# Optimization experiments

Measured on AMD Instinct MI355X. Metric: run time of the kernel, lower is better.

Reference implementation:

```python
import jax, jax.numpy as jnp
import numpy as np

N = 50000      # nodes
E = 800000     # edges (avg degree 16)
IN = 128       # in_features
H = 4          # num_heads
OUT = 32       # out_features per head
NEG_SLOPE = 0.2


def setup_inputs() -> dict:
    key = jax.random.key(0)
    k1, k2, k3, k4 = jax.random.split(key, 4)
    h = jax.random.normal(k1, (N, IN), dtype=jnp.float32)
    edge_index = jax.random.randint(k2, (2, E), 0, N, dtype=jnp.int32)
    # xavier-ish init scales
    W = jax.random.normal(k3, (H, IN, OUT), dtype=jnp.float32) * np.float32(np.sqrt(2.0 / (IN + OUT)))
    a = jax.random.normal(k4, (H, 2 * OUT), dtype=jnp.float32) * np.float32(np.sqrt(2.0 / (2 * OUT)))
    return {"h": h, "edge_index": edge_index, "W": W, "a": a}


def reference(h, edge_index, W, a):
    src, dst = edge_index[0], edge_index[1]
    # project per head: [N, H, OUT]
    h_proj = jnp.einsum('ni,hio->nho', h, W)
    # score = leaky_relu(a . [Wh_src || Wh_dst]) ; split a to avoid materializing the concat
    a_src, a_dst = a[:, :OUT], a[:, OUT:]
    s_src = jnp.einsum('nho,ho->nh', h_proj, a_src)   # [N, H]
    s_dst = jnp.einsum('nho,ho->nh', h_proj, a_dst)   # [N, H]
    score = jax.nn.leaky_relu(s_src[src] + s_dst[dst], negative_slope=NEG_SLOPE)  # [E, H]
    # sparse softmax over incoming edges of each dst node
    smax = jax.ops.segment_max(score, dst, num_segments=N)          # [N, H]
    smax = jnp.where(jnp.isfinite(smax), smax, jnp.float32(-1e9))   # nodes with no in-edges
    score_exp = jnp.exp(score - smax[dst])                          # [E, H]
    denom = jax.ops.segment_sum(score_exp, dst, num_segments=N)     # [N, H]
    denom = jnp.maximum(denom, jnp.float32(1e-16))
    alpha = score_exp / denom[dst]                                  # [E, H]
    # weighted aggregation (dropout is identity in eval mode)
    h_src = h_proj[src]                                             # [E, H, OUT]
    h_out = jax.ops.segment_sum(alpha[:, :, None] * h_src, dst, num_segments=N)  # [N, H, OUT]
    h_out = h_out.reshape(N, H * OUT)  # concat=True
    return jax.nn.elu(h_out)
```

## Files before the change

kernel.cpp:

```cpp
#include <hip/hip_runtime.h>

#define NEG_SLOPE 0.2f

typedef __attribute__((ext_vector_type(8))) short short8;
typedef __attribute__((ext_vector_type(4))) float floatx4;

__device__ __forceinline__ unsigned f2bf(float x) {
  unsigned u = __float_as_uint(x);
  unsigned r = ((u >> 16) & 1u) + 0x7fffu;
  return (u + r) >> 16;
}
__device__ __forceinline__ float bf2f(unsigned hi16) {
  return __uint_as_float(hi16 << 16);
}

__global__ __launch_bounds__(256) void k_prep(const float* __restrict__ W,
                                              uint4* __restrict__ gWf) {
  const int u = blockIdx.x * 256 + threadIdx.x;
  if (u >= 2048) return;
  int ln = u & 63;
  int kc = (u >> 6) & 3;
  int ct = u >> 8;
  int n = ct * 16 + (ln & 15);
  int kb = kc * 32 + (ln >> 4) * 8;
  int head = n >> 5;
  const float* src = W + head * 4096 + (size_t)kb * 32 + (n & 31);
  unsigned hi[4], lo[4];
#pragma unroll
  for (int jj = 0; jj < 4; ++jj) {
    float w0 = src[(2 * jj) * 32];
    float w1 = src[(2 * jj + 1) * 32];
    unsigned h0 = f2bf(w0), h1 = f2bf(w1);
    unsigned l0 = f2bf(w0 - bf2f(h0)), l1 = f2bf(w1 - bf2f(h1));
    hi[jj] = h0 | (h1 << 16);
    lo[jj] = l0 | (l1 << 16);
  }
  gWf[u] = make_uint4(hi[0], hi[1], hi[2], hi[3]);
  gWf[2048 + u] = make_uint4(lo[0], lo[1], lo[2], lo[3]);
}

__global__ __launch_bounds__(256) void k_gemm(const float* __restrict__ h,
                                              const uint4* __restrict__ gWf,
                                              const float* __restrict__ a,
                                              unsigned short* __restrict__ hp16,
                                              float* __restrict__ ssrc,
                                              float* __restrict__ sdst, int N) {
  __shared__ unsigned lds_u[16384];
  const int tid = threadIdx.x;
  const int lane = tid & 63;
  const int wv = tid >> 6;
  const int quad = lane >> 4;
  const int l16 = lane & 15;

  for (int u = tid; u < 4096; u += 256)
    *(uint4*)&lds_u[u * 4] = gWf[u];

  const int row0 = blockIdx.x * 64;
  const int r = row0 + wv * 16 + l16;
  short8 Ah[4], Al[4];
#pragma unroll
  for (int kc = 0; kc < 4; ++kc) {
    float v[8];
    if (r < N) {
      float4 fa = *(const float4*)&h[(size_t)r * 128 + kc * 32 + quad * 8];
      float4 fb = *(const float4*)&h[(size_t)r * 128 + kc * 32 + quad * 8 + 4];
      v[0] = fa.x; v[1] = fa.y; v[2] = fa.z; v[3] = fa.w;
      v[4] = fb.x; v[5] = fb.y; v[6] = fb.z; v[7] = fb.w;
    } else {
#pragma unroll
      for (int j = 0; j < 8; ++j) v[j] = 0.f;
    }
#pragma unroll
    for (int j = 0; j < 8; ++j) {
      unsigned hi = f2bf(v[j]);
      Ah[kc][j] = (short)hi;
      Al[kc][j] = (short)f2bf(v[j] - bf2f(hi));
    }
  }
  __syncthreads();

  floatx4 C[8];
#pragma unroll
  for (int ct = 0; ct < 8; ++ct) {
    floatx4 c = {0.f, 0.f, 0.f, 0.f};
#pragma unroll
    for (int kc = 0; kc < 4; ++kc) {
      int bidx = ((ct * 4 + kc) * 64 + lane) * 4;
      short8 Bh, Bl;
      *(uint4*)&Bh = *(const uint4*)&lds_u[bidx];
      *(uint4*)&Bl = *(const uint4*)&lds_u[8192 + bidx];
      c = __builtin_amdgcn_mfma_f32_16x16x32_bf16(Ah[kc], Bh, c, 0, 0, 0);
      c = __builtin_amdgcn_mfma_f32_16x16x32_bf16(Al[kc], Bh, c, 0, 0, 0);
      c = __builtin_amdgcn_mfma_f32_16x16x32_bf16(Ah[kc], Bl, c, 0, 0, 0);
    }
    C[ct] = c;
  }
  __syncthreads();

  float* epi = (float*)lds_u;
#pragma unroll
  for (int ct = 0; ct < 8; ++ct) {
#pragma unroll
    for (int reg = 0; reg < 4; ++reg) {
      int rr = wv * 16 + quad * 4 + reg;
      epi[rr * 132 + ct * 16 + l16] = C[ct][reg];
    }
  }
  __syncthreads();

  const int row_l = tid >> 2;
  const int hh = tid & 3;
  const int rg = row0 + row_l;
  if (rg < N) {
    const float* rowp = &epi[row_l * 132 + hh * 32];
    float ss = 0.f, sd = 0.f;
    unsigned pka[16];
#pragma unroll
    for (int e = 0; e < 8; ++e) {
      float4 c4 = *(const float4*)&rowp[e * 4];
      float4 as = *(const float4*)&a[hh * 64 + e * 4];
      float4 ad = *(const float4*)&a[hh * 64 + 32 + e * 4];
      ss += c4.x * as.x + c4.y * as.y + c4.z * as.z + c4.w * as.w;
      sd += c4.x * ad.x + c4.y * ad.y + c4.z * ad.z + c4.w * ad.w;
      pka[e * 2] = f2bf(c4.x) | (f2bf(c4.y) << 16);
      pka[e * 2 + 1] = f2bf(c4.z) | (f2bf(c4.w) << 16);
    }
    unsigned short* dst = &hp16[(size_t)rg * 128 + hh * 32];
    *(uint4*)(dst) = make_uint4(pka[0], pka[1], pka[2], pka[3]);
    *(uint4*)(dst + 8) = make_uint4(pka[4], pka[5], pka[6], pka[7]);
    *(uint4*)(dst + 16) = make_uint4(pka[8], pka[9], pka[10], pka[11]);
    *(uint4*)(dst + 24) = make_uint4(pka[12], pka[13], pka[14], pka[15]);
    ssrc[(size_t)rg * 4 + hh] = ss;
    sdst[(size_t)rg * 4 + hh] = sd;
  }
}

__global__ __launch_bounds__(256) void k_count(const int* __restrict__ ei,
                                               int* __restrict__ gcntT,
                                               int E, int NB1, int NB2) {
  __shared__ int cnt[256];
  const int tid = threadIdx.x;
  const int e0 = blockIdx.x * 4096;
  for (int i = tid; i < NB2; i += 256) cnt[i] = 0;
  __syncthreads();
#pragma unroll
  for (int j = 0; j < 16; ++j) {
    int e = e0 + j * 256 + tid;
    if (e < E) atomicAdd(&cnt[ei[E + e] >> 8], 1);
  }
  __syncthreads();
  for (int i = tid; i < NB2; i += 256)
    gcntT[(size_t)i * NB1 + blockIdx.x] = cnt[i];
}

__global__ __launch_bounds__(256) void k_scan_col(int* __restrict__ gcntT,
                                                  int* __restrict__ btot, int NB1) {
  __shared__ int lds[256];
  const int tid = threadIdx.x;
  int* col = gcntT + (size_t)blockIdx.x * NB1;
  int carry = 0;
  for (int base = 0; base < NB1; base += 256) {
    int i = base + tid;
    int v = (i < NB1) ? col[i] : 0;
    lds[tid] = v;
    __syncthreads();
    for (int off = 1; off < 256; off <<= 1) {
      int t = (tid >= off) ? lds[tid - off] : 0;
      __syncthreads();
      lds[tid] += t;
      __syncthreads();
    }
    if (i < NB1) col[i] = carry + lds[tid] - v;
    carry += lds[255];
    __syncthreads();
  }
  if (tid == 0) btot[blockIdx.x] = carry;
}

__global__ __launch_bounds__(256) void k_scan_bk(const int* __restrict__ btot,
                                                 int* __restrict__ bbase, int NB2, int E) {
  __shared__ int lds[256];
  const int tid = threadIdx.x;
  int s = (tid < NB2) ? btot[tid] : 0;
  lds[tid] = s;
  __syncthreads();
  for (int off = 1; off < 256; off <<= 1) {
    int t = (tid >= off) ? lds[tid - off] : 0;
    __syncthreads();
    lds[tid] += t;
    __syncthreads();
  }
  if (tid < NB2) {
    bbase[tid] = lds[tid] - s;
    if (tid == NB2 - 1) bbase[NB2] = E;
  }
}

__global__ __launch_bounds__(256) void k_bin(const int* __restrict__ ei,
                                             const int* __restrict__ gcntT,
                                             const int* __restrict__ bbase,
                                             uint2* __restrict__ gpairs,
                                             int E, int NB1, int NB2) {
  __shared__ uint2 stage[4096];
  __shared__ int cnt[256], start[256], cur[256], gbase[256];
  const int tid = threadIdx.x;
  const int e0 = blockIdx.x * 4096;
  for (int i = tid; i < NB2; i += 256) cnt[i] = 0;
  __syncthreads();
  int sarr[16], darr[16];
#pragma unroll
  for (int j = 0; j < 16; ++j) {
    int e = e0 + j * 256 + tid;
    if (e < E) {
      sarr[j] = ei[e];
      darr[j] = ei[E + e];
      atomicAdd(&cnt[darr[j] >> 8], 1);
    } else {
      darr[j] = -1;
    }
  }
  __syncthreads();
  {
    int s = (tid < NB2) ? cnt[tid] : 0;
    __shared__ int lds[256];
    lds[tid] = s;
    __syncthreads();
    for (int off = 1; off < 256; off <<= 1) {
      int t = (tid >= off) ? lds[tid - off] : 0;
      __syncthreads();
      lds[tid] += t;
      __syncthreads();
    }
    if (tid < NB2) {
      start[tid] = lds[tid] - s;
      cur[tid] = lds[tid] - s;
      gbase[tid] = gcntT[(size_t)tid * NB1 + blockIdx.x] + bbase[tid];
    }
  }
  __syncthreads();
#pragma unroll
  for (int j = 0; j < 16; ++j) {
    if (darr[j] >= 0) {
      int b = darr[j] >> 8;
      int pos = atomicAdd(&cur[b], 1);
      stage[pos] = make_uint2((unsigned)sarr[j], (unsigned)darr[j]);
    }
  }
  __syncthreads();
  const int total = start[NB2 - 1] + cnt[NB2 - 1];
  for (int u = tid; u < total; u += 256) {
    uint2 pr = stage[u];
    int b = (int)(pr.y >> 8);
    gpairs[gbase[b] + (u - start[b])] = pr;
  }
}

__global__ __launch_bounds__(256) void k_build(const int* __restrict__ bbase,
                                               const uint2* __restrict__ gpairs,
                                               int* __restrict__ csr_src,
                                               int* __restrict__ offs, int N) {
  __shared__ int cnt2[256], start2[256], cur2[256];
  __shared__ int srcsort[8192];
  const int tid = threadIdx.x;
  const int b = blockIdx.x;
  const int base = bbase[b];
  const int size = bbase[b + 1] - base;
  const int d0 = b << 8;
  const int ndst = min(256, N - d0);
  cnt2[tid] = 0;
  __syncthreads();
  for (int u = tid; u < size; u += 256)
    atomicAdd(&cnt2[(int)gpairs[base + u].y - d0], 1);
  __syncthreads();
  {
    int s = cnt2[tid];
    __shared__ int lds[256];
    lds[tid] = s;
    __syncthreads();
    for (int off = 1; off < 256; off <<= 1) {
      int t = (tid >= off) ? lds[tid - off] : 0;
      __syncthreads();
      lds[tid] += t;
      __syncthreads();
    }
    start2[tid] = lds[tid] - s;
    cur2[tid] = lds[tid] - s;
  }
  __syncthreads();
  for (int u = tid; u < size; u += 256) {
    uint2 pr = gpairs[base + u];
    int pos = atomicAdd(&cur2[(int)pr.y - d0], 1);
    srcsort[pos] = (int)pr.x;
  }
  __syncthreads();
  for (int u = tid; u < size; u += 256) csr_src[base + u] = srcsort[u];
  if (tid < ndst) offs[d0 + tid] = base + start2[tid] + cnt2[tid];
}

__global__ __launch_bounds__(256) void k_agg(const int* __restrict__ offs,
                                             const int* __restrict__ csr_src,
                                             const float* __restrict__ ssrc,
                                             const float* __restrict__ sdst,
                                             const uint4* __restrict__ hp4,
                                             float* __restrict__ out, int N) {
  const int t = blockIdx.x * 256 + threadIdx.x;
  const int d = t >> 4;
  if (d >= N) return;
  const int l = threadIdx.x & 15;
  const int hh = l >> 2;
  const int beg = (d == 0) ? 0 : offs[d - 1];
  const int end = offs[d];
  const float sdh = sdst[(size_t)d * 4 + hh];

  float den0 = 0.f, den1 = 0.f;
  float acc[8];
#pragma unroll
  for (int j = 0; j < 8; ++j) acc[j] = 0.f;

  int p = beg;
  for (; p + 1 < end; p += 2) {
    int s0 = csr_src[p];
    int s1 = csr_src[p + 1];
    float sc0 = ssrc[(size_t)s0 * 4 + hh] + sdh;
    float sc1 = ssrc[(size_t)s1 * 4 + hh] + sdh;
    uint4 v0 = hp4[(size_t)s0 * 16 + l];
    uint4 v1 = hp4[(size_t)s1 * 16 + l];
    sc0 = sc0 >= 0.f ? sc0 : NEG_SLOPE * sc0;
    sc1 = sc1 >= 0.f ? sc1 : NEG_SLOPE * sc1;
    float w0 = __expf(sc0);
    float w1 = __expf(sc1);
    den0 += w0;
    den1 += w1;
    acc[0] = fmaf(w0, bf2f(v0.x & 0xffffu), acc[0]);
    acc[1] = fmaf(w0, bf2f(v0.x >> 16), acc[1]);
    acc[2] = fmaf(w0, bf2f(v0.y & 0xffffu), acc[2]);
    acc[3] = fmaf(w0, bf2f(v0.y >> 16), acc[3]);
    acc[4] = fmaf(w0, bf2f(v0.z & 0xffffu), acc[4]);
    acc[5] = fmaf(w0, bf2f(v0.z >> 16), acc[5]);
    acc[6] = fmaf(w0, bf2f(v0.w & 0xffffu), acc[6]);
    acc[7] = fmaf(w0, bf2f(v0.w >> 16), acc[7]);
    acc[0] = fmaf(w1, bf2f(v1.x & 0xffffu), acc[0]);
    acc[1] = fmaf(w1, bf2f(v1.x >> 16), acc[1]);
    acc[2] = fmaf(w1, bf2f(v1.y & 0xffffu), acc[2]);
    acc[3] = fmaf(w1, bf2f(v1.y >> 16), acc[3]);
    acc[4] = fmaf(w1, bf2f(v1.z & 0xffffu), acc[4]);
    acc[5] = fmaf(w1, bf2f(v1.z >> 16), acc[5]);
    acc[6] = fmaf(w1, bf2f(v1.w & 0xffffu), acc[6]);
    acc[7] = fmaf(w1, bf2f(v1.w >> 16), acc[7]);
  }
  if (p < end) {
    int s0 = csr_src[p];
    float sc0 = ssrc[(size_t)s0 * 4 + hh] + sdh;
    uint4 v0 = hp4[(size_t)s0 * 16 + l];
    sc0 = sc0 >= 0.f ? sc0 : NEG_SLOPE * sc0;
    float w0 = __expf(sc0);
    den0 += w0;
    acc[0] = fmaf(w0, bf2f(v0.x & 0xffffu), acc[0]);
    acc[1] = fmaf(w0, bf2f(v0.x >> 16), acc[1]);
    acc[2] = fmaf(w0, bf2f(v0.y & 0xffffu), acc[2]);
    acc[3] = fmaf(w0, bf2f(v0.y >> 16), acc[3]);
    acc[4] = fmaf(w0, bf2f(v0.z & 0xffffu), acc[4]);
    acc[5] = fmaf(w0, bf2f(v0.z >> 16), acc[5]);
    acc[6] = fmaf(w0, bf2f(v0.w & 0xffffu), acc[6]);
    acc[7] = fmaf(w0, bf2f(v0.w >> 16), acc[7]);
  }
  float rden = 1.f / fmaxf(den0 + den1, 1e-16f);
  float o[8];
#pragma unroll
  for (int j = 0; j < 8; ++j) {
    float x = acc[j] * rden;
    o[j] = x > 0.f ? x : expm1f(x);
  }
  float* dst = &out[(size_t)d * 128 + l * 8];
  *(float4*)dst = make_float4(o[0], o[1], o[2], o[3]);
  *(float4*)(dst + 4) = make_float4(o[4], o[5], o[6], o[7]);
}

extern "C" void kernel_launch(void* const* d_in, const int* in_sizes, int n_in,
                              void* d_out, int out_size, void* d_ws, size_t ws_size,
                              hipStream_t stream) {
  const float* h = (const float*)d_in[0];
  const int* ei = (const int*)d_in[1];
  const float* W = (const float*)d_in[2];
  const float* a = (const float*)d_in[3];
  float* out = (float*)d_out;
  const int N = in_sizes[0] / 128;
  const int E = in_sizes[1] / 2;
  const int NB2 = (N + 255) >> 8;
  const int NB1 = (E + 4095) / 4096;

  char* ws = (char*)d_ws;
  uint4* gWf = (uint4*)ws;
  unsigned short* hp16 = (unsigned short*)(gWf + 4096);
  uint2* gpairs = (uint2*)(hp16 + (size_t)N * 128);
  float* ssrc = (float*)(gpairs + (size_t)E);
  float* sdst = ssrc + (size_t)N * 4;
  int* gcntT = (int*)(sdst + (size_t)N * 4);
  int* btot = gcntT + (size_t)NB2 * NB1;
  int* bbase = btot + NB2;
  int* offs = bbase + NB2 + 1;
  int* csr_src = offs + N;

  k_prep<<<8, 256, 0, stream>>>(W, gWf);
  k_gemm<<<(N + 63) / 64, 256, 0, stream>>>(h, gWf, a, hp16, ssrc, sdst, N);
  k_count<<<NB1, 256, 0, stream>>>(ei, gcntT, E, NB1, NB2);
  k_scan_col<<<NB2, 256, 0, stream>>>(gcntT, btot, NB1);
  k_scan_bk<<<1, 256, 0, stream>>>(btot, bbase, NB2, E);
  k_bin<<<NB1, 256, 0, stream>>>(ei, gcntT, bbase, gpairs, E, NB1, NB2);
  k_build<<<NB2, 256, 0, stream>>>(bbase, gpairs, csr_src, offs, N);
  k_agg<<<(N * 16 + 255) / 256, 256, 0, stream>>>(offs, csr_src, ssrc, sdst,
                                                  (const uint4*)hp16, out, N);
}
```

Baseline: 167.3 us.

## Fuse edge counting into GEMM, inline bucket scan, unroll aggregation by four

The per-bucket destination counting moves into the first NB1 blocks of the GEMM kernel, and the single-block bucket-base scan kernel is removed. k_bin and k_build now each recompute that scan redundantly from btot. This cuts two launches and their serialization gaps, at the cost of extra scan work in every block and a longer GEMM prologue in some blocks. The aggregation loop is unrolled from two to four edges, with four denominator partials, to put more independent gathers in flight.

```diff
diff --git a/kernel.cpp b/kernel.cpp
--- a/kernel.cpp
+++ b/kernel.cpp
@@ -42,11 +42,30 @@
 __global__ __launch_bounds__(256) void k_gemm(const float* __restrict__ h,
                                               const uint4* __restrict__ gWf,
                                               const float* __restrict__ a,
+                                              const int* __restrict__ ei,
                                               unsigned short* __restrict__ hp16,
                                               float* __restrict__ ssrc,
-                                              float* __restrict__ sdst, int N) {
+                                              float* __restrict__ sdst,
+                                              int* __restrict__ gcntT,
+                                              int N, int E, int NB1, int NB2) {
   __shared__ unsigned lds_u[16384];
+  __shared__ int cnt[256];
   const int tid = threadIdx.x;
+
+  if (blockIdx.x < NB1) {
+    for (int i = tid; i < NB2; i += 256) cnt[i] = 0;
+    __syncthreads();
+    const int e0 = blockIdx.x * 4096;
+#pragma unroll
+    for (int j = 0; j < 16; ++j) {
+      int e = e0 + j * 256 + tid;
+      if (e < E) atomicAdd(&cnt[ei[E + e] >> 8], 1);
+    }
+    __syncthreads();
+    for (int i = tid; i < NB2; i += 256)
+      gcntT[(size_t)i * NB1 + blockIdx.x] = cnt[i];
+  }
+
   const int lane = tid & 63;
   const int wv = tid >> 6;
   const int quad = lane >> 4;
@@ -133,24 +152,6 @@
     ssrc[(size_t)rg * 4 + hh] = ss;
     sdst[(size_t)rg * 4 + hh] = sd;
   }
-}
-
-__global__ __launch_bounds__(256) void k_count(const int* __restrict__ ei,
-                                               int* __restrict__ gcntT,
-                                               int E, int NB1, int NB2) {
-  __shared__ int cnt[256];
-  const int tid = threadIdx.x;
-  const int e0 = blockIdx.x * 4096;
-  for (int i = tid; i < NB2; i += 256) cnt[i] = 0;
-  __syncthreads();
-#pragma unroll
-  for (int j = 0; j < 16; ++j) {
-    int e = e0 + j * 256 + tid;
-    if (e < E) atomicAdd(&cnt[ei[E + e] >> 8], 1);
-  }
-  __syncthreads();
-  for (int i = tid; i < NB2; i += 256)
-    gcntT[(size_t)i * NB1 + blockIdx.x] = cnt[i];
 }
 
 __global__ __launch_bounds__(256) void k_scan_col(int* __restrict__ gcntT,
@@ -177,34 +178,26 @@
   if (tid == 0) btot[blockIdx.x] = carry;
 }
 
-__global__ __launch_bounds__(256) void k_scan_bk(const int* __restrict__ btot,
-                                                 int* __restrict__ bbase, int NB2, int E) {
-  __shared__ int lds[256];
-  const int tid = threadIdx.x;
-  int s = (tid < NB2) ? btot[tid] : 0;
-  lds[tid] = s;
-  __syncthreads();
-  for (int off = 1; off < 256; off <<= 1) {
-    int t = (tid >= off) ? lds[tid - off] : 0;
-    __syncthreads();
-    lds[tid] += t;
-    __syncthreads();
-  }
-  if (tid < NB2) {
-    bbase[tid] = lds[tid] - s;
-    if (tid == NB2 - 1) bbase[NB2] = E;
-  }
-}
-
 __global__ __launch_bounds__(256) void k_bin(const int* __restrict__ ei,
                                              const int* __restrict__ gcntT,
-                                             const int* __restrict__ bbase,
+                                             const int* __restrict__ btot,
                                              uint2* __restrict__ gpairs,
                                              int E, int NB1, int NB2) {
   __shared__ uint2 stage[4096];
   __shared__ int cnt[256], start[256], cur[256], gbase[256];
+  __shared__ int lds[256];
   const int tid = threadIdx.x;
   const int e0 = blockIdx.x * 4096;
+  int bt = (tid < NB2) ? btot[tid] : 0;
+  lds[tid] = bt;
+  __syncthreads();
+  for (int off = 1; off < 256; off <<= 1) {
+    int t = (tid >= off) ? lds[tid - off] : 0;
+    __syncthreads();
+    lds[tid] += t;
+    __syncthreads();
+  }
+  const int bbase_t = lds[tid] - bt;
   for (int i = tid; i < NB2; i += 256) cnt[i] = 0;
   __syncthreads();
   int sarr[16], darr[16];
@@ -222,7 +215,6 @@
   __syncthreads();
   {
     int s = (tid < NB2) ? cnt[tid] : 0;
-    __shared__ int lds[256];
     lds[tid] = s;
     __syncthreads();
     for (int off = 1; off < 256; off <<= 1) {
@@ -234,7 +226,7 @@
     if (tid < NB2) {
       start[tid] = lds[tid] - s;
       cur[tid] = lds[tid] - s;
-      gbase[tid] = gcntT[(size_t)tid * NB1 + blockIdx.x] + bbase[tid];
+      gbase[tid] = gcntT[(size_t)tid * NB1 + blockIdx.x] + bbase_t;
     }
   }
   __syncthreads();
@@ -255,26 +247,40 @@
   }
 }
 
-__global__ __launch_bounds__(256) void k_build(const int* __restrict__ bbase,
+__global__ __launch_bounds__(256) void k_build(const int* __restrict__ btot,
                                                const uint2* __restrict__ gpairs,
                                                int* __restrict__ csr_src,
-                                               int* __restrict__ offs, int N) {
+                                               int* __restrict__ offs, int N, int NB2) {
   __shared__ int cnt2[256], start2[256], cur2[256];
+  __shared__ int lds[256];
+  __shared__ int bshare[2];
   __shared__ int srcsort[8192];
   const int tid = threadIdx.x;
   const int b = blockIdx.x;
-  const int base = bbase[b];
-  const int size = bbase[b + 1] - base;
+  int bt = (tid < NB2) ? btot[tid] : 0;
+  lds[tid] = bt;
+  __syncthreads();
+  for (int off = 1; off < 256; off <<= 1) {
+    int t = (tid >= off) ? lds[tid - off] : 0;
+    __syncthreads();
+    lds[tid] += t;
+    __syncthreads();
+  }
+  if (tid == b) {
+    bshare[0] = lds[tid] - bt;
+    bshare[1] = bt;
+  }
+  cnt2[tid] = 0;
+  __syncthreads();
+  const int base = bshare[0];
+  const int size = bshare[1];
   const int d0 = b << 8;
   const int ndst = min(256, N - d0);
-  cnt2[tid] = 0;
-  __syncthreads();
   for (int u = tid; u < size; u += 256)
     atomicAdd(&cnt2[(int)gpairs[base + u].y - d0], 1);
   __syncthreads();
   {
     int s = cnt2[tid];
-    __shared__ int lds[256];
     lds[tid] = s;
     __syncthreads();
     for (int off = 1; off < 256; off <<= 1) {
@@ -312,25 +318,46 @@
   const int end = offs[d];
   const float sdh = sdst[(size_t)d * 4 + hh];
 
-  float den0 = 0.f, den1 = 0.f;
+  float den[4] = {0.f, 0.f, 0.f, 0.f};
   float acc[8];
 #pragma unroll
   for (int j = 0; j < 8; ++j) acc[j] = 0.f;
 
   int p = beg;
-  for (; p + 1 < end; p += 2) {
+  for (; p + 3 < end; p += 4) {
+    int s[4];
+    float sc[4];
+    uint4 v[4];
+#pragma unroll
+    for (int q = 0; q < 4; ++q) s[q] = csr_src[p + q];
+#pragma unroll
+    for (int q = 0; q < 4; ++q) {
+      sc[q] = ssrc[(size_t)s[q] * 4 + hh] + sdh;
+      v[q] = hp4[(size_t)s[q] * 16 + l];
+    }
+#pragma unroll
+    for (int q = 0; q < 4; ++q) {
+      float x = sc[q];
+      x = x >= 0.f ? x : NEG_SLOPE * x;
+      float w = __expf(x);
+      den[q] += w;
+      acc[0] = fmaf(w, bf2f(v[q].x & 0xffffu), acc[0]);
+      acc[1] = fmaf(w, bf2f(v[q].x >> 16), acc[1]);
+      acc[2] = fmaf(w, bf2f(v[q].y & 0xffffu), acc[2]);
+      acc[3] = fmaf(w, bf2f(v[q].y >> 16), acc[3]);
+      acc[4] = fmaf(w, bf2f(v[q].z & 0xffffu), acc[4]);
+      acc[5] = fmaf(w, bf2f(v[q].z >> 16), acc[5]);
+      acc[6] = fmaf(w, bf2f(v[q].w & 0xffffu), acc[6]);
+      acc[7] = fmaf(w, bf2f(v[q].w >> 16), acc[7]);
+    }
+  }
+  for (; p < end; ++p) {
     int s0 = csr_src[p];
-    int s1 = csr_src[p + 1];
     float sc0 = ssrc[(size_t)s0 * 4 + hh] + sdh;
-    float sc1 = ssrc[(size_t)s1 * 4 + hh] + sdh;
     uint4 v0 = hp4[(size_t)s0 * 16 + l];
-    uint4 v1 = hp4[(size_t)s1 * 16 + l];
     sc0 = sc0 >= 0.f ? sc0 : NEG_SLOPE * sc0;
-    sc1 = sc1 >= 0.f ? sc1 : NEG_SLOPE * sc1;
     float w0 = __expf(sc0);
-    float w1 = __expf(sc1);
-    den0 += w0;
-    den1 += w1;
+    den[0] += w0;
     acc[0] = fmaf(w0, bf2f(v0.x & 0xffffu), acc[0]);
     acc[1] = fmaf(w0, bf2f(v0.x >> 16), acc[1]);
     acc[2] = fmaf(w0, bf2f(v0.y & 0xffffu), acc[2]);
@@ -339,32 +366,8 @@
     acc[5] = fmaf(w0, bf2f(v0.z >> 16), acc[5]);
     acc[6] = fmaf(w0, bf2f(v0.w & 0xffffu), acc[6]);
     acc[7] = fmaf(w0, bf2f(v0.w >> 16), acc[7]);
-    acc[0] = fmaf(w1, bf2f(v1.x & 0xffffu), acc[0]);
-    acc[1] = fmaf(w1, bf2f(v1.x >> 16), acc[1]);
-    acc[2] = fmaf(w1, bf2f(v1.y & 0xffffu), acc[2]);
-    acc[3] = fmaf(w1, bf2f(v1.y >> 16), acc[3]);
-    acc[4] = fmaf(w1, bf2f(v1.z & 0xffffu), acc[4]);
-    acc[5] = fmaf(w1, bf2f(v1.z >> 16), acc[5]);
-    acc[6] = fmaf(w1, bf2f(v1.w & 0xffffu), acc[6]);
-    acc[7] = fmaf(w1, bf2f(v1.w >> 16), acc[7]);
-  }
-  if (p < end) {
-    int s0 = csr_src[p];
-    float sc0 = ssrc[(size_t)s0 * 4 + hh] + sdh;
-    uint4 v0 = hp4[(size_t)s0 * 16 + l];
-    sc0 = sc0 >= 0.f ? sc0 : NEG_SLOPE * sc0;
-    float w0 = __expf(sc0);
-    den0 += w0;
-    acc[0] = fmaf(w0, bf2f(v0.x & 0xffffu), acc[0]);
-    acc[1] = fmaf(w0, bf2f(v0.x >> 16), acc[1]);
-    acc[2] = fmaf(w0, bf2f(v0.y & 0xffffu), acc[2]);
-    acc[3] = fmaf(w0, bf2f(v0.y >> 16), acc[3]);
-    acc[4] = fmaf(w0, bf2f(v0.z & 0xffffu), acc[4]);
-    acc[5] = fmaf(w0, bf2f(v0.z >> 16), acc[5]);
-    acc[6] = fmaf(w0, bf2f(v0.w & 0xffffu), acc[6]);
-    acc[7] = fmaf(w0, bf2f(v0.w >> 16), acc[7]);
-  }
-  float rden = 1.f / fmaxf(den0 + den1, 1e-16f);
+  }
+  float rden = 1.f / fmaxf((den[0] + den[1]) + (den[2] + den[3]), 1e-16f);
   float o[8];
 #pragma unroll
   for (int j = 0; j < 8; ++j) {
@@ -397,17 +400,15 @@
   float* sdst = ssrc + (size_t)N * 4;
   int* gcntT = (int*)(sdst + (size_t)N * 4);
   int* btot = gcntT + (size_t)NB2 * NB1;
-  int* bbase = btot + NB2;
-  int* offs = bbase + NB2 + 1;
+  int* offs = btot + NB2;
   int* csr_src = offs + N;
 
   k_prep<<<8, 256, 0, stream>>>(W, gWf);
-  k_gemm<<<(N + 63) / 64, 256, 0, stream>>>(h, gWf, a, hp16, ssrc, sdst, N);
-  k_count<<<NB1, 256, 0, stream>>>(ei, gcntT, E, NB1, NB2);
+  k_gemm<<<(N + 63) / 64, 256, 0, stream>>>(h, gWf, a, ei, hp16, ssrc, sdst,
+                                            gcntT, N, E, NB1, NB2);
   k_scan_col<<<NB2, 256, 0, stream>>>(gcntT, btot, NB1);
-  k_scan_bk<<<1, 256, 0, stream>>>(btot, bbase, NB2, E);
-  k_bin<<<NB1, 256, 0, stream>>>(ei, gcntT, bbase, gpairs, E, NB1, NB2);
-  k_build<<<NB2, 256, 0, stream>>>(bbase, gpairs, csr_src, offs, N);
+  k_bin<<<NB1, 256, 0, stream>>>(ei, gcntT, btot, gpairs, E, NB1, NB2);
+  k_build<<<NB2, 256, 0, stream>>>(btot, gpairs, csr_src, offs, N, NB2);
   k_agg<<<(N * 16 + 255) / 256, 256, 0, stream>>>(offs, csr_src, ssrc, sdst,
                                                   (const uint4*)hp16, out, N);
 }
```

New measurement: 163.6 us. 1.02x faster.
